# Kernel tuning notes

Hardware: AMD Instinct MI355X
Metric: run time of the kernel (lower is better)

The kernel has to match this reference:

```python
import jax, jax.numpy as jnp
import numpy as np

NUM_ELMT = 64
INPUT_DIM = 16
BOUND = 50.0
MESH_RATIO = 1.2
N_POINTS = 1_048_576


def _build_mesh():
    m = NUM_ELMT
    one_step = BOUND * (MESH_RATIO - 1.0) / (MESH_RATIO ** (m / 2) - 1.0)
    idx = np.arange(-m / 2, m / 2 + 1)
    mesh = (MESH_RATIO ** np.abs(idx) - 1.0) / (MESH_RATIO - 1.0) * one_step * np.sign(idx)
    mesh_norm = (mesh + BOUND) / (2.0 * BOUND)
    mesh_norm = np.concatenate([[0.0], mesh_norm[1:-1], [1.0]]).astype(np.float32)
    elmt_size = (mesh_norm[1:] - mesh_norm[:-1]).astype(np.float32)
    return jnp.asarray(mesh_norm), jnp.asarray(elmt_size)


def setup_inputs() -> dict:
    key = jax.random.key(0)
    k1, k2 = jax.random.split(key)
    x = jax.random.uniform(k1, (N_POINTS, INPUT_DIM), jnp.float32, minval=-BOUND, maxval=BOUND)
    pdj = jnp.ones((N_POINTS, 1), jnp.float32)
    sldj = jnp.zeros((N_POINTS, 1), jnp.float32)
    log_p = 0.1 * jax.random.normal(k2, (NUM_ELMT - 1, INPUT_DIM), jnp.float32)
    mesh_norm, elmt_size = _build_mesh()
    return {"x": x, "pdj": pdj, "sldj": sldj, "log_p": log_p,
            "mesh_norm": mesh_norm, "elmt_size": elmt_size}


def _normalize_pdf(log_p, elmt_size):
    # elmt_size: (M,) -> (M,1) column, log_p: (M-1, D)
    es = elmt_size[:, None]
    ep = jnp.exp(log_p)
    px = ep * (es[:-1] + es[1:]) / 2.0
    px = ep * (1.0 - es[0]) / jnp.sum(px, axis=0, keepdims=True)
    p0 = jnp.ones((1, log_p.shape[1]), log_p.dtype)
    pdf_norm = jnp.concatenate([p0, px, p0], axis=0)            # (M+1, D)
    cell = (pdf_norm[:-1] + pdf_norm[1:]) / 2.0 * es            # (M, D)
    # F_ref[i] = sum(cell[:i]); single cumsum instead of the O(M^2) torch loop
    F_ref = jnp.concatenate([jnp.zeros_like(p0), jnp.cumsum(cell, axis=0)[:-1]], axis=0)  # (M, D)
    return pdf_norm, F_ref


def reference(x, pdj, sldj, log_p, mesh_norm, elmt_size):
    pdf_norm, F_ref = _normalize_pdf(log_p, elmt_size)
    xn = (x + BOUND) / (2.0 * BOUND)                            # (N, D) in [0,1]
    k = jnp.searchsorted(mesh_norm, xn, side='left')            # (N, D), torch right=False
    cover = (k != 0) & (k != NUM_ELMT + 1)
    k = jnp.clip(k, 1, NUM_ELMT)
    km1 = k - 1
    v1 = jnp.take_along_axis(pdf_norm, km1, axis=0)             # pdf at lower node
    v2 = jnp.take_along_axis(pdf_norm, k, axis=0)               # pdf at upper node
    xmodi = xn - mesh_norm[km1]                                 # offset inside element
    h = elmt_size[km1]                                          # element width
    F_pre = jnp.take_along_axis(F_ref, km1, axis=0)             # CDF at lower node
    y = jnp.where(cover, F_pre + xmodi * xmodi * 0.5 * (v2 - v1) / h + xmodi * v1, xn)
    abs_det = jnp.where(cover, xmodi * (v2 - v1) / h + v1, 1.0)
    pdj_out = pdj * jnp.prod(abs_det, axis=-1, keepdims=True)
    sldj_out = sldj + jnp.sum(jnp.log(abs_det), axis=-1, keepdims=True)
    x_out = y * 2.0 * BOUND - BOUND
    return (x_out, pdj_out, sldj_out)
```

## Files before the change

### kernel.cpp

```cpp
#include <hip/hip_runtime.h>
#include <math.h>
#include <stdint.h>


namespace {
constexpr int DIM = 16;
constexpr int ME  = 64;
constexpr float BOUNDF = 50.0f;
constexpr float K1      = 6.8164378f;
constexpr float INV_L2R = 3.8017840f;
constexpr int NBIN = 66;
constexpr int ROWF = 68;
constexpr int COEF_FLOATS = NBIN * ROWF;
constexpr int EP_BASE = COEF_FLOATS - 63 * DIM;
}

__global__ __launch_bounds__(256, 8) void nll_kernel(
    const float* __restrict__ x,
    const float* __restrict__ pdj,
    const float* __restrict__ sldj,
    const float* __restrict__ log_p,
    const float* __restrict__ mesh_norm,
    float* __restrict__ out,
    int npts, int npairs)
{
  __shared__ __align__(16) float co[COEF_FLOATS];
  __shared__ float s_mesh[ME + 1];

  const int tid = threadIdx.x;

  if (tid <= ME) s_mesh[tid] = mesh_norm[tid];
  for (int i = tid; i < 63 * DIM; i += 256)
    co[EP_BASE + i] = __expf(log_p[i]);
  __syncthreads();

  const int wv = tid >> 6, lane = tid & 63;
  float epv[4];
#pragma unroll
  for (int i = 0; i < 4; ++i)
    epv[i] = (lane < 63) ? co[EP_BASE + lane * DIM + (4 * wv + i)] : 0.f;
  const float mj  = s_mesh[lane];
  const float mj1 = s_mesh[lane + 1];
  const float mj2 = s_mesh[(lane + 2 > ME) ? ME : (lane + 2)];
  const float es0 = s_mesh[1] - s_mesh[0];
  __syncthreads();

  const float h = mj1 - mj;
#pragma unroll
  for (int i = 0; i < 4; ++i) {
    const int d = 4 * wv + i;
    const float ep = epv[i];
    float ss = (lane < 63) ? ep * (mj2 - mj) : 0.f;
    ss += __shfl_xor(ss, 1);  ss += __shfl_xor(ss, 2);  ss += __shfl_xor(ss, 4);
    ss += __shfl_xor(ss, 8);  ss += __shfl_xor(ss, 16); ss += __shfl_xor(ss, 32);
    const float scale = (1.0f - es0) / (0.5f * ss);
    const float cur = (lane < 63) ? ep * scale : 1.0f;
    float prev = __shfl_up(cur, 1);
    if (lane == 0) prev = 1.0f;
    const float cell = (prev + cur) * 0.5f * h;
    float v = cell, o;
    o = __shfl_up(v, 1);  if (lane >= 1)  v += o;
    o = __shfl_up(v, 2);  if (lane >= 2)  v += o;
    o = __shfl_up(v, 4);  if (lane >= 4)  v += o;
    o = __shfl_up(v, 8);  if (lane >= 8)  v += o;
    o = __shfl_up(v, 16); if (lane >= 16) v += o;
    o = __shfl_up(v, 32); if (lane >= 32) v += o;
    const float F = v - cell;
    const float A = 0.5f * (cur - prev) / h;
    const float B = fmaf(-(A + A), mj, prev);
    const float D = fmaf(mj, fmaf(mj, A, -prev), F);
    *reinterpret_cast<float4*>(&co[(lane + 1) * ROWF + 4 * d]) = make_float4(A, B, D, A + A);
  }
  if (tid < 32) {
    const int row = (tid >> 4) ? (NBIN - 1) : 0;
    const int d = tid & 15;
    *reinterpret_cast<float4*>(&co[row * ROWF + 4 * d]) = make_float4(0.f, 1.f, 0.f, 0.f);
  }
  __syncthreads();

  const int tpg = gridDim.x * blockDim.x;
  const float4* __restrict__ x4 = reinterpret_cast<const float4*>(x);
  float4* __restrict__ out4 = reinterpret_cast<float4*>(out);
  const int np16 = npts * DIM;

  int t = blockIdx.x * blockDim.x + tid;
  if (t >= npairs) return;

#define ISSUE_TILE(TT, XA, XB, PS)                                            \
  {                                                                           \
    const float4* xs_ = x4 + 2 * (TT);                                        \
    const float* ss_ = (((TT) & 1) ? sldj : pdj) + ((TT) >> 1);               \
    asm volatile("global_load_dwordx4 %0, %1, off" : "=v"(XA) : "v"(xs_));    \
    asm volatile("global_load_dwordx4 %0, %1, off" : "=v"(XB) : "v"(xs_ + 1));\
    asm volatile("global_load_dword %0, %1, off"   : "=v"(PS) : "v"(ss_));    \
  }

#define COMPUTE_TILE(TT, XA, XB, PS)                                          \
  {                                                                           \
    const int p_  = (TT) >> 1;                                                \
    const int hh_ = (TT) & 1;                                                 \
    const int dbase_ = hh_ << 5;                                              \
    const float vals_[8] = {(XA).x, (XA).y, (XA).z, (XA).w,                   \
                            (XB).x, (XB).y, (XB).z, (XB).w};                  \
    float xn_[8]; int idx_[8];                                                \
    _Pragma("unroll")                                                         \
    for (int j = 0; j < 8; ++j) {                                             \
      const float val_ = vals_[j];                                            \
      xn_[j] = fmaf(val_, 0.01f, 0.5f);                                       \
      const float u_ = fmaf(fabsf(val_), K1, 1.0f);                           \
      const float n_ = __log2f(u_) * INV_L2R;                                 \
      int k_ = 32 + (int)ceilf(copysignf(n_, val_));                          \
      k_ = k_ < 0 ? 0 : (k_ > NBIN - 1 ? NBIN - 1 : k_);                      \
      idx_[j] = k_ * ROWF + dbase_ + (j << 2);                                \
    }                                                                         \
    float4 cf_[8];                                                            \
    _Pragma("unroll")                                                         \
    for (int j = 0; j < 8; ++j)                                               \
      cf_[j] = *reinterpret_cast<const float4*>(&co[idx_[j]]);                \
    float yv_[8], dt_[8];                                                     \
    _Pragma("unroll")                                                         \
    for (int j = 0; j < 8; ++j) {                                             \
      const float z_ = xn_[j];                                                \
      yv_[j] = fmaf(fmaf(z_, fmaf(z_, cf_[j].x, cf_[j].y), cf_[j].z),         \
                    2.0f * BOUNDF, -BOUNDF);                                  \
      dt_[j] = fmaf(z_, cf_[j].w, cf_[j].y);                                  \
    }                                                                         \
    const float prod_ = ((dt_[0] * dt_[1]) * (dt_[2] * dt_[3])) *             \
                        ((dt_[4] * dt_[5]) * (dt_[6] * dt_[7]));              \
    out4[2 * (TT)]     = make_float4(yv_[0], yv_[1], yv_[2], yv_[3]);         \
    out4[2 * (TT) + 1] = make_float4(yv_[4], yv_[5], yv_[6], yv_[7]);         \
    const float full_ = prod_ * __shfl_xor(prod_, 1);                         \
    const float res_  = hh_ ? ((PS) + __logf(full_)) : ((PS) * full_);        \
    out[np16 + hh_ * npts + p_] = res_;                                       \
  }

#define WAIT_PINNED()                                                         \
  asm volatile("s_waitcnt vmcnt(6)" ::: "memory");                            \
  __builtin_amdgcn_sched_barrier(0);

  float4 a0 = x4[2 * t], a1 = x4[2 * t + 1];
  float aps = (t & 1) ? sldj[t >> 1] : pdj[t >> 1];
  float4 b0, b1; float bps;
  {
    const int tn = (t + tpg < npairs) ? t + tpg : t;
    ISSUE_TILE(tn, b0, b1, bps);
  }

  for (;;) {
    COMPUTE_TILE(t, a0, a1, aps);
    int t1 = t + tpg;
    if (t1 >= npairs) break;
    {
      const int tn = (t1 + tpg < npairs) ? t1 + tpg : t1;
      ISSUE_TILE(tn, a0, a1, aps);
    }
    WAIT_PINNED();

    COMPUTE_TILE(t1, b0, b1, bps);
    t = t1 + tpg;
    if (t >= npairs) break;
    {
      const int tn = (t + tpg < npairs) ? t + tpg : t;
      ISSUE_TILE(tn, b0, b1, bps);
    }
    WAIT_PINNED();
  }
#undef ISSUE_TILE
#undef COMPUTE_TILE
#undef WAIT_PINNED
}

extern "C" void kernel_launch(void* const* d_in, const int* in_sizes, int n_in,
                              void* d_out, int out_size, void* d_ws, size_t ws_size,
                              hipStream_t stream) {
  const float* x    = (const float*)d_in[0];
  const float* pdj  = (const float*)d_in[1];
  const float* sldj = (const float*)d_in[2];
  const float* lp   = (const float*)d_in[3];
  const float* mesh = (const float*)d_in[4];
  float* out = (float*)d_out;

  const int npts   = in_sizes[0] / DIM;
  const int npairs = npts * 2;
  const int block  = 256;
  int grid = 2048;
  const int needed = (npairs + block - 1) / block;
  if (needed < grid) grid = needed;

  hipLaunchKernelGGL(nll_kernel, dim3(grid), dim3(block), 0, stream,
                     x, pdj, sldj, lp, mesh, out, npts, npairs);
}
```

Measured before the change: 32.68 us.

## Issue all four tiles' loads up front when grid exactly covers work

Replaces the double-buffered inline-asm load pipeline with a specialized path that loads all four tiles per thread at once and then computes them, taken when the pair count equals four times the thread count. The goal is maximum memory-level parallelism and no waitcnt stalls between tiles. The min-blocks-per-SM launch bound is removed, so more registers can be used at the cost of occupancy. A generic strided loop serves as the fallback.

```diff
diff --git a/kernel.cpp b/kernel.cpp
--- a/kernel.cpp
+++ b/kernel.cpp
@@ -15,7 +15,7 @@
 constexpr int EP_BASE = COEF_FLOATS - 63 * DIM;
 }
 
-__global__ __launch_bounds__(256, 8) void nll_kernel(
+__global__ __launch_bounds__(256) void nll_kernel(
     const float* __restrict__ x,
     const float* __restrict__ pdj,
     const float* __restrict__ sldj,
@@ -83,23 +83,11 @@
   float4* __restrict__ out4 = reinterpret_cast<float4*>(out);
   const int np16 = npts * DIM;
 
-  int t = blockIdx.x * blockDim.x + tid;
-  if (t >= npairs) return;
+  const int t0 = blockIdx.x * blockDim.x + tid;
 
-#define ISSUE_TILE(TT, XA, XB, PS)                                            \
+#define COMPUTE_TILE(TT, DBASE, HH, XA, XB, PS)                               \
   {                                                                           \
-    const float4* xs_ = x4 + 2 * (TT);                                        \
-    const float* ss_ = (((TT) & 1) ? sldj : pdj) + ((TT) >> 1);               \
-    asm volatile("global_load_dwordx4 %0, %1, off" : "=v"(XA) : "v"(xs_));    \
-    asm volatile("global_load_dwordx4 %0, %1, off" : "=v"(XB) : "v"(xs_ + 1));\
-    asm volatile("global_load_dword %0, %1, off"   : "=v"(PS) : "v"(ss_));    \
-  }
-
-#define COMPUTE_TILE(TT, XA, XB, PS)                                          \
-  {                                                                           \
-    const int p_  = (TT) >> 1;                                                \
-    const int hh_ = (TT) & 1;                                                 \
-    const int dbase_ = hh_ << 5;                                              \
+    const int p_ = (TT) >> 1;                                                 \
     const float vals_[8] = {(XA).x, (XA).y, (XA).z, (XA).w,                   \
                             (XB).x, (XB).y, (XB).z, (XB).w};                  \
     float xn_[8]; int idx_[8];                                                \
@@ -111,7 +99,7 @@
       const float n_ = __log2f(u_) * INV_L2R;                                 \
       int k_ = 32 + (int)ceilf(copysignf(n_, val_));                          \
       k_ = k_ < 0 ? 0 : (k_ > NBIN - 1 ? NBIN - 1 : k_);                      \
-      idx_[j] = k_ * ROWF + dbase_ + (j << 2);                                \
+      idx_[j] = k_ * ROWF + (DBASE) + (j << 2);                               \
     }                                                                         \
     float4 cf_[8];                                                            \
     _Pragma("unroll")                                                         \
@@ -130,44 +118,38 @@
     out4[2 * (TT)]     = make_float4(yv_[0], yv_[1], yv_[2], yv_[3]);         \
     out4[2 * (TT) + 1] = make_float4(yv_[4], yv_[5], yv_[6], yv_[7]);         \
     const float full_ = prod_ * __shfl_xor(prod_, 1);                         \
-    const float res_  = hh_ ? ((PS) + __logf(full_)) : ((PS) * full_);        \
-    out[np16 + hh_ * npts + p_] = res_;                                       \
+    const float res_  = (HH) ? ((PS) + __logf(full_)) : ((PS) * full_);       \
+    out[np16 + (HH) * npts + p_] = res_;                                      \
   }
 
-#define WAIT_PINNED()                                                         \
-  asm volatile("s_waitcnt vmcnt(6)" ::: "memory");                            \
-  __builtin_amdgcn_sched_barrier(0);
+  if (npairs == 4 * tpg) {
+    const int t1 = t0 + tpg, t2 = t1 + tpg, t3 = t2 + tpg;
+    const int hh = t0 & 1;
+    const int dbase = hh << 5;
+    const float* __restrict__ sb = hh ? sldj : pdj;
 
-  float4 a0 = x4[2 * t], a1 = x4[2 * t + 1];
-  float aps = (t & 1) ? sldj[t >> 1] : pdj[t >> 1];
-  float4 b0, b1; float bps;
-  {
-    const int tn = (t + tpg < npairs) ? t + tpg : t;
-    ISSUE_TILE(tn, b0, b1, bps);
+    const float4 a0 = x4[2 * t0], a1 = x4[2 * t0 + 1];
+    const float4 b0 = x4[2 * t1], b1 = x4[2 * t1 + 1];
+    const float4 c0 = x4[2 * t2], c1 = x4[2 * t2 + 1];
+    const float4 d0 = x4[2 * t3], d1 = x4[2 * t3 + 1];
+    const float ap = sb[t0 >> 1], bp = sb[t1 >> 1];
+    const float cp = sb[t2 >> 1], dp = sb[t3 >> 1];
+    __builtin_amdgcn_sched_barrier(0);
+
+    COMPUTE_TILE(t0, dbase, hh, a0, a1, ap);
+    COMPUTE_TILE(t1, dbase, hh, b0, b1, bp);
+    COMPUTE_TILE(t2, dbase, hh, c0, c1, cp);
+    COMPUTE_TILE(t3, dbase, hh, d0, d1, dp);
+  } else {
+    for (int t = t0; t < npairs; t += tpg) {
+      const int hh = t & 1;
+      const int dbase = hh << 5;
+      const float4 xa = x4[2 * t], xb = x4[2 * t + 1];
+      const float ps = hh ? sldj[t >> 1] : pdj[t >> 1];
+      COMPUTE_TILE(t, dbase, hh, xa, xb, ps);
+    }
   }
-
-  for (;;) {
-    COMPUTE_TILE(t, a0, a1, aps);
-    int t1 = t + tpg;
-    if (t1 >= npairs) break;
-    {
-      const int tn = (t1 + tpg < npairs) ? t1 + tpg : t1;
-      ISSUE_TILE(tn, a0, a1, aps);
-    }
-    WAIT_PINNED();
-
-    COMPUTE_TILE(t1, b0, b1, bps);
-    t = t1 + tpg;
-    if (t >= npairs) break;
-    {
-      const int tn = (t + tpg < npairs) ? t + tpg : t;
-      ISSUE_TILE(tn, b0, b1, bps);
-    }
-    WAIT_PINNED();
-  }
-#undef ISSUE_TILE
 #undef COMPUTE_TILE
-#undef WAIT_PINNED
 }
 
 extern "C" void kernel_launch(void* const* d_in, const int* in_sizes, int n_in,
```

New measurement: 36.84 us. 12.7% more time.
